# Performance work log

Hardware: AMD Instinct MI355X
Metric: run time of the kernel (lower is better)

## Reference

```python
import jax, jax.numpy as jnp
import numpy as np

N_NODES = 8192
N_EDGES = 524288
D_IN = 256
D_OUT = 256


def setup_inputs() -> dict:
    key = jax.random.key(0)
    ks = jax.random.split(key, 8)
    h = jax.random.normal(ks[0], (N_NODES, D_IN), dtype=jnp.float32)
    # Xavier-uniform-like scale for weights
    s = (6.0 / (D_IN + D_OUT)) ** 0.5
    W = jax.random.uniform(ks[1], (D_IN, D_OUT), jnp.float32, -s, s)
    Wq = jax.random.uniform(ks[2], (D_IN, D_OUT), jnp.float32, -s, s)
    bq = jnp.zeros((D_OUT,), jnp.float32)
    Wk = jax.random.uniform(ks[3], (D_IN, D_OUT), jnp.float32, -s, s)
    bk = jnp.zeros((D_OUT,), jnp.float32)
    senders = jax.random.randint(ks[4], (N_EDGES,), 0, N_NODES, dtype=jnp.int64 if jax.config.jax_enable_x64 else jnp.int32)
    receivers = jax.random.randint(ks[5], (N_EDGES,), 0, N_NODES, dtype=jnp.int64 if jax.config.jax_enable_x64 else jnp.int32)
    return {"h": h, "W": W, "Wq": Wq, "bq": bq, "Wk": Wk, "bk": bk,
            "senders": senders, "receivers": receivers}


def reference(h, W, Wq, bq, Wk, bk, senders, receivers):
    # Projected node features: (N, D_OUT)
    h_proj = jnp.dot(h, W)
    # Dense attention logits a = q @ k^T: (N, N), as in the original module
    q = jnp.dot(h, Wq) + bq
    k = jnp.dot(h, Wk) + bk
    a = jnp.dot(q, k.T)
    # Gather per-edge messages and attention weights, weight, scatter-add
    messages = h_proj[senders] * a[senders, receivers][:, None]  # (E, D_OUT)
    aggregated = jax.ops.segment_sum(messages, receivers, num_segments=h.shape[0])
    return jax.nn.relu(aggregated)
```

## Files before the change

### kernel.cpp

```cpp
#include <hip/hip_runtime.h>
#include <stdint.h>

typedef unsigned short u16;
typedef unsigned int u32;
typedef short v8s __attribute__((ext_vector_type(8)));
typedef float v4f __attribute__((ext_vector_type(4)));

#define N_NODES 8192
#define N_EDGES 524288
#define DFEAT 256
#define PAD 160
#define PADE 176

static __device__ __forceinline__ float bflo(u32 u) { return __uint_as_float(u << 16); }
static __device__ __forceinline__ float bfhi(u32 u) { return __uint_as_float(u & 0xffff0000u); }
static __device__ __forceinline__ u16 f2bf(float f) {
    u32 u = __float_as_uint(f);
    u32 r = (u + 0x7fffu + ((u >> 16) & 1u)) >> 16;
    return (u16)r;
}

__global__ void prep(const float* __restrict__ w0, const float* __restrict__ w1,
                     const float* __restrict__ w2,
                     const int* __restrict__ recv, const int* __restrict__ send,
                     u16* __restrict__ wt,
                     int* __restrict__ cnt, int* __restrict__ es_pad) {
    __shared__ u16 t[64][65];
    int b = blockIdx.x;
    if (b < 2048) {
        int e = b * 256 + threadIdx.x;
        int r = recv[e];
        int pos = atomicAdd(&cnt[r], 1);
        if (pos < PAD) es_pad[r * PAD + pos] = send[e];
    } else {
        int bb = b - 2048;
        int region = bb >> 4;
        int tile = bb & 15;
        int k0 = (tile >> 2) * 64, n0 = (tile & 3) * 64;
        const float* w = (region == 0) ? w0 : ((region == 1) ? w1 : w2);
        int tx = threadIdx.x & 63, ty = threadIdx.x >> 6;
#pragma unroll
        for (int it = 0; it < 16; it++) {
            int row = it * 4 + ty;
            t[row][tx] = f2bf(w[(k0 + row) * 256 + n0 + tx]);
        }
        __syncthreads();
        u16* o = wt + region * 65536;
#pragma unroll
        for (int it = 0; it < 16; it++) {
            int row = it * 4 + ty;
            o[(n0 + row) * 256 + k0 + tx] = t[tx][row];
        }
    }
}

__global__ __launch_bounds__(256) void gemm_proj(
    const float* __restrict__ h, const u16* __restrict__ wt,
    const float* __restrict__ bq, const float* __restrict__ bk,
    u16* __restrict__ hproj, u16* __restrict__ qb, u16* __restrict__ kb) {
    int wave = threadIdx.x >> 6;
    int lane = threadIdx.x & 63;
    int lm = lane & 15;
    int lq = lane >> 4;
    int m0 = blockIdx.x * 64 + wave * 16;
    int region = blockIdx.y >> 2;
    int n0b = (blockIdx.y & 3) * 64;
    const u16* wtr = wt + region * 65536;

    v4f acc[4];
#pragma unroll
    for (int nt = 0; nt < 4; nt++) acc[nt] = (v4f){0.f, 0.f, 0.f, 0.f};

    const float* arow = h + (m0 + lm) * 256 + lq * 8;
#pragma unroll
    for (int k0 = 0; k0 < 256; k0 += 32) {
        float4 u0 = *(const float4*)(arow + k0);
        float4 u1 = *(const float4*)(arow + k0 + 4);
        v8s a;
        a[0] = (short)f2bf(u0.x); a[1] = (short)f2bf(u0.y);
        a[2] = (short)f2bf(u0.z); a[3] = (short)f2bf(u0.w);
        a[4] = (short)f2bf(u1.x); a[5] = (short)f2bf(u1.y);
        a[6] = (short)f2bf(u1.z); a[7] = (short)f2bf(u1.w);
#pragma unroll
        for (int nt = 0; nt < 4; nt++) {
            v8s b = *(const v8s*)(wtr + (n0b + nt * 16 + lm) * 256 + k0 + lq * 8);
            acc[nt] = __builtin_amdgcn_mfma_f32_16x16x32_bf16(a, b, acc[nt], 0, 0, 0);
        }
    }

    u16* outp = (region == 0) ? hproj : ((region == 1) ? qb : kb);
    const float* bias = (region == 1) ? bq : ((region == 2) ? bk : nullptr);
#pragma unroll
    for (int nt = 0; nt < 4; nt++) {
        int n = n0b + nt * 16 + lm;
        float bv = bias ? bias[n] : 0.f;
#pragma unroll
        for (int i = 0; i < 4; i++) {
            int m = m0 + lq * 4 + i;
            outp[m * 256 + n] = f2bf(acc[nt][i] + bv);
        }
    }
}

__global__ __launch_bounds__(64) void edge_score(
    const u16* __restrict__ qb, const u16* __restrict__ kb,
    const int* __restrict__ cnt, const int* __restrict__ es_pad,
    float* __restrict__ ea_pad) {
    int lane = threadIdx.x;
    int r = blockIdx.x;
    int lm = lane & 15, lq = lane >> 4;
    int n = min(cnt[r], PAD);
    int base = r * PAD;
    int obase = r * PADE;

    v8s kf[8];
    const u16* krow = kb + r * 256 + lq * 8;
#pragma unroll
    for (int t = 0; t < 8; t++) kf[t] = *(const v8s*)(krow + t * 32);

    for (int c0 = 0; c0 < n; c0 += 16) {
        int jq = c0 + lm;
        if (jq >= n) jq = n - 1;
        int sq = es_pad[base + jq];
        const u16* qrow = qb + (long)sq * 256 + lq * 8;
        v4f acc = (v4f){0.f, 0.f, 0.f, 0.f};
#pragma unroll
        for (int t = 0; t < 8; t++) {
            v8s av = *(const v8s*)(qrow + t * 32);
            acc = __builtin_amdgcn_mfma_f32_16x16x32_bf16(av, kf[t], acc, 0, 0, 0);
        }
        if (lm == 0) {
#pragma unroll
            for (int i = 0; i < 4; i++) {
                int row = c0 + lq * 4 + i;
                ea_pad[obase + row] = acc[i];
            }
        }
    }
}

__global__ __launch_bounds__(64) void edge_aggregate(
    const u16* __restrict__ hpb, const int* __restrict__ cnt,
    const int* __restrict__ es_pad, const float* __restrict__ ea_pad,
    float* __restrict__ out) {
    int lane = threadIdx.x;
    int r = blockIdx.x;
    int lh = lane & 31, half = lane >> 5;
    int n = min(cnt[r], PAD);
    int base = r * PAD;
    int obase = r * PADE;

    float a[8];
#pragma unroll
    for (int i = 0; i < 8; i++) a[i] = 0.f;

#pragma unroll 4
    for (int t = half; t < n; t += 2) {
        int s = es_pad[base + t];
        float p = ea_pad[obase + t];
        uint4 hu = *(const uint4*)(hpb + (long)s * 256 + lh * 8);
        a[0] += p * bflo(hu.x); a[1] += p * bfhi(hu.x);
        a[2] += p * bflo(hu.y); a[3] += p * bfhi(hu.y);
        a[4] += p * bflo(hu.z); a[5] += p * bfhi(hu.z);
        a[6] += p * bflo(hu.w); a[7] += p * bfhi(hu.w);
    }

#pragma unroll
    for (int i = 0; i < 8; i++) a[i] += __shfl_xor(a[i], 32, 64);

    if (half == 0) {
        float4 o0, o1;
        o0.x = fmaxf(a[0], 0.f); o0.y = fmaxf(a[1], 0.f);
        o0.z = fmaxf(a[2], 0.f); o0.w = fmaxf(a[3], 0.f);
        o1.x = fmaxf(a[4], 0.f); o1.y = fmaxf(a[5], 0.f);
        o1.z = fmaxf(a[6], 0.f); o1.w = fmaxf(a[7], 0.f);
        float* op = out + r * 256 + lh * 8;
        *(float4*)op = o0;
        *(float4*)(op + 4) = o1;
    }
}

extern "C" void kernel_launch(void* const* d_in, const int* in_sizes, int n_in,
                              void* d_out, int out_size, void* d_ws, size_t ws_size,
                              hipStream_t stream) {
    const float* h  = (const float*)d_in[0];
    const float* W  = (const float*)d_in[1];
    const float* Wq = (const float*)d_in[2];
    const float* bq = (const float*)d_in[3];
    const float* Wk = (const float*)d_in[4];
    const float* bk = (const float*)d_in[5];
    const int* senders   = (const int*)d_in[6];
    const int* receivers = (const int*)d_in[7];
    float* out = (float*)d_out;

    char* ws = (char*)d_ws;
    u16* wt     = (u16*)ws;
    u16* hproj  = (u16*)(ws + 393216);
    u16* qb     = hproj + N_NODES * DFEAT;
    u16* kb     = qb + N_NODES * DFEAT;
    int* cnt    = (int*)(kb + N_NODES * DFEAT);
    int* es_pad = cnt + N_NODES;
    float* ea_pad = (float*)(es_pad + N_NODES * PAD);

    hipMemsetAsync(cnt, 0, N_NODES * sizeof(int), stream);
    prep<<<2096, 256, 0, stream>>>(W, Wq, Wk, receivers, senders, wt, cnt, es_pad);
    gemm_proj<<<dim3(128, 12), 256, 0, stream>>>(h, wt, bq, bk, hproj, qb, kb);
    edge_score<<<N_NODES, 64, 0, stream>>>(qb, kb, cnt, es_pad, ea_pad);
    edge_aggregate<<<N_NODES, 64, 0, stream>>>(hproj, cnt, es_pad, ea_pad, out);
}
```

Baseline: 188.4 us.

## Restructure projection GEMM and split edge kernels across more waves

The projection GEMM now has each wave convert its 16-row h slice to bf16 once, keep it in registers, and loop over all three weight matrices and all 256 output columns. This removes the repeated fp32 loads and conversions of h across column blocks, but the grid shrinks to 256 blocks of 128 threads. Edge scoring now splits each receiver's edges across two blocks, and aggregation uses two waves per receiver, combining their partial sums through shared memory. The added parallelism in the edge kernels costs an extra k-row reload per block and a block-level sync.

```diff
diff --git a/kernel.cpp b/kernel.cpp
--- a/kernel.cpp
+++ b/kernel.cpp
@@ -54,7 +54,7 @@
     }
 }
 
-__global__ __launch_bounds__(256) void gemm_proj(
+__global__ __launch_bounds__(128) void gemm_proj(
     const float* __restrict__ h, const u16* __restrict__ wt,
     const float* __restrict__ bq, const float* __restrict__ bk,
     u16* __restrict__ hproj, u16* __restrict__ qb, u16* __restrict__ kb) {
@@ -62,42 +62,40 @@
     int lane = threadIdx.x & 63;
     int lm = lane & 15;
     int lq = lane >> 4;
-    int m0 = blockIdx.x * 64 + wave * 16;
-    int region = blockIdx.y >> 2;
-    int n0b = (blockIdx.y & 3) * 64;
-    const u16* wtr = wt + region * 65536;
-
-    v4f acc[4];
-#pragma unroll
-    for (int nt = 0; nt < 4; nt++) acc[nt] = (v4f){0.f, 0.f, 0.f, 0.f};
-
+    int m0 = blockIdx.x * 32 + wave * 16;
+
+    v8s af[8];
     const float* arow = h + (m0 + lm) * 256 + lq * 8;
 #pragma unroll
-    for (int k0 = 0; k0 < 256; k0 += 32) {
-        float4 u0 = *(const float4*)(arow + k0);
-        float4 u1 = *(const float4*)(arow + k0 + 4);
+    for (int t = 0; t < 8; t++) {
+        float4 u0 = *(const float4*)(arow + t * 32);
+        float4 u1 = *(const float4*)(arow + t * 32 + 4);
         v8s a;
         a[0] = (short)f2bf(u0.x); a[1] = (short)f2bf(u0.y);
         a[2] = (short)f2bf(u0.z); a[3] = (short)f2bf(u0.w);
         a[4] = (short)f2bf(u1.x); a[5] = (short)f2bf(u1.y);
         a[6] = (short)f2bf(u1.z); a[7] = (short)f2bf(u1.w);
-#pragma unroll
-        for (int nt = 0; nt < 4; nt++) {
-            v8s b = *(const v8s*)(wtr + (n0b + nt * 16 + lm) * 256 + k0 + lq * 8);
-            acc[nt] = __builtin_amdgcn_mfma_f32_16x16x32_bf16(a, b, acc[nt], 0, 0, 0);
-        }
-    }
-
-    u16* outp = (region == 0) ? hproj : ((region == 1) ? qb : kb);
-    const float* bias = (region == 1) ? bq : ((region == 2) ? bk : nullptr);
-#pragma unroll
-    for (int nt = 0; nt < 4; nt++) {
-        int n = n0b + nt * 16 + lm;
-        float bv = bias ? bias[n] : 0.f;
-#pragma unroll
-        for (int i = 0; i < 4; i++) {
-            int m = m0 + lq * 4 + i;
-            outp[m * 256 + n] = f2bf(acc[nt][i] + bv);
+        af[t] = a;
+    }
+
+#pragma unroll
+    for (int region = 0; region < 3; region++) {
+        const u16* wtr = wt + region * 65536;
+        u16* outp = (region == 0) ? hproj : ((region == 1) ? qb : kb);
+        const float* bias = (region == 1) ? bq : ((region == 2) ? bk : nullptr);
+        for (int nt = 0; nt < 16; nt++) {
+            const u16* bp = wtr + (nt * 16 + lm) * 256 + lq * 8;
+            v4f acc = (v4f){0.f, 0.f, 0.f, 0.f};
+#pragma unroll
+            for (int t = 0; t < 8; t++) {
+                v8s b = *(const v8s*)(bp + t * 32);
+                acc = __builtin_amdgcn_mfma_f32_16x16x32_bf16(af[t], b, acc, 0, 0, 0);
+            }
+            int n = nt * 16 + lm;
+            float bv = bias ? bias[n] : 0.f;
+#pragma unroll
+            for (int i = 0; i < 4; i++)
+                outp[(m0 + lq * 4 + i) * 256 + n] = f2bf(acc[i] + bv);
         }
     }
 }
@@ -107,7 +105,7 @@
     const int* __restrict__ cnt, const int* __restrict__ es_pad,
     float* __restrict__ ea_pad) {
     int lane = threadIdx.x;
-    int r = blockIdx.x;
+    int r = blockIdx.x >> 1, part = blockIdx.x & 1;
     int lm = lane & 15, lq = lane >> 4;
     int n = min(cnt[r], PAD);
     int base = r * PAD;
@@ -118,7 +116,7 @@
 #pragma unroll
     for (int t = 0; t < 8; t++) kf[t] = *(const v8s*)(krow + t * 32);
 
-    for (int c0 = 0; c0 < n; c0 += 16) {
+    for (int c0 = part * 16; c0 < n; c0 += 32) {
         int jq = c0 + lm;
         if (jq >= n) jq = n - 1;
         int sq = es_pad[base + jq];
@@ -131,19 +129,19 @@
         }
         if (lm == 0) {
 #pragma unroll
-            for (int i = 0; i < 4; i++) {
-                int row = c0 + lq * 4 + i;
-                ea_pad[obase + row] = acc[i];
-            }
-        }
-    }
-}
-
-__global__ __launch_bounds__(64) void edge_aggregate(
+            for (int i = 0; i < 4; i++)
+                ea_pad[obase + c0 + lq * 4 + i] = acc[i];
+        }
+    }
+}
+
+__global__ __launch_bounds__(128) void edge_aggregate(
     const u16* __restrict__ hpb, const int* __restrict__ cnt,
     const int* __restrict__ es_pad, const float* __restrict__ ea_pad,
     float* __restrict__ out) {
-    int lane = threadIdx.x;
+    __shared__ float comb[64][9];
+    int wave = threadIdx.x >> 6;
+    int lane = threadIdx.x & 63;
     int r = blockIdx.x;
     int lh = lane & 31, half = lane >> 5;
     int n = min(cnt[r], PAD);
@@ -154,8 +152,8 @@
 #pragma unroll
     for (int i = 0; i < 8; i++) a[i] = 0.f;
 
-#pragma unroll 4
-    for (int t = half; t < n; t += 2) {
+#pragma unroll 2
+    for (int t = wave * 2 + half; t < n; t += 4) {
         int s = es_pad[base + t];
         float p = ea_pad[obase + t];
         uint4 hu = *(const uint4*)(hpb + (long)s * 256 + lh * 8);
@@ -165,18 +163,26 @@
         a[6] += p * bflo(hu.w); a[7] += p * bfhi(hu.w);
     }
 
-#pragma unroll
-    for (int i = 0; i < 8; i++) a[i] += __shfl_xor(a[i], 32, 64);
-
-    if (half == 0) {
-        float4 o0, o1;
-        o0.x = fmaxf(a[0], 0.f); o0.y = fmaxf(a[1], 0.f);
-        o0.z = fmaxf(a[2], 0.f); o0.w = fmaxf(a[3], 0.f);
-        o1.x = fmaxf(a[4], 0.f); o1.y = fmaxf(a[5], 0.f);
-        o1.z = fmaxf(a[6], 0.f); o1.w = fmaxf(a[7], 0.f);
-        float* op = out + r * 256 + lh * 8;
-        *(float4*)op = o0;
-        *(float4*)(op + 4) = o1;
+    if (wave == 1) {
+#pragma unroll
+        for (int i = 0; i < 8; i++) comb[lane][i] = a[i];
+    }
+    __syncthreads();
+    if (wave == 0) {
+#pragma unroll
+        for (int i = 0; i < 8; i++) a[i] += comb[lane][i];
+#pragma unroll
+        for (int i = 0; i < 8; i++) a[i] += __shfl_xor(a[i], 32, 64);
+        if (half == 0) {
+            float4 o0, o1;
+            o0.x = fmaxf(a[0], 0.f); o0.y = fmaxf(a[1], 0.f);
+            o0.z = fmaxf(a[2], 0.f); o0.w = fmaxf(a[3], 0.f);
+            o1.x = fmaxf(a[4], 0.f); o1.y = fmaxf(a[5], 0.f);
+            o1.z = fmaxf(a[6], 0.f); o1.w = fmaxf(a[7], 0.f);
+            float* op = out + r * 256 + lh * 8;
+            *(float4*)op = o0;
+            *(float4*)(op + 4) = o1;
+        }
     }
 }
 
@@ -204,7 +210,7 @@
 
     hipMemsetAsync(cnt, 0, N_NODES * sizeof(int), stream);
     prep<<<2096, 256, 0, stream>>>(W, Wq, Wk, receivers, senders, wt, cnt, es_pad);
-    gemm_proj<<<dim3(128, 12), 256, 0, stream>>>(h, wt, bq, bk, hproj, qb, kb);
-    edge_score<<<N_NODES, 64, 0, stream>>>(qb, kb, cnt, es_pad, ea_pad);
-    edge_aggregate<<<N_NODES, 64, 0, stream>>>(hproj, cnt, es_pad, ea_pad, out);
-}
+    gemm_proj<<<256, 128, 0, stream>>>(h, wt, bq, bk, hproj, qb, kb);
+    edge_score<<<N_NODES * 2, 64, 0, stream>>>(qb, kb, cnt, es_pad, ea_pad);
+    edge_aggregate<<<N_NODES, 128, 0, stream>>>(hproj, cnt, es_pad, ea_pad, out);
+}
```

Result: slower. 221.7 us (+17.7%).
